# Kernel tuning notes

Measured on AMD Instinct MI355X. Metric: run time of the kernel, lower is better.

Reference implementation:

```python
import jax, jax.numpy as jnp
import numpy as np

B, T, A, F_, D, H = 8, 128, 6, 64, 64, 4  # batch, time, antennas, subcarriers, d_model, heads


def setup_inputs() -> dict:
    key = jax.random.key(0)
    ks = jax.random.split(key, 10)
    d = D
    s = 1.0 / np.sqrt(d)
    return {
        "x": jax.random.normal(ks[0], (B, T, A, F_), jnp.float32),
        "embed_w": jax.random.normal(ks[1], (d, 1), jnp.float32) * 0.5,
        "embed_b": jax.random.normal(ks[2], (d,), jnp.float32) * 0.1,
        "in_proj_w": jax.random.normal(ks[3], (3 * d, d), jnp.float32) * s,
        "in_proj_b": jax.random.normal(ks[4], (3 * d,), jnp.float32) * 0.1,
        "out_proj_w": jax.random.normal(ks[5], (d, d), jnp.float32) * s,
        "out_proj_b": jax.random.normal(ks[6], (d,), jnp.float32) * 0.1,
        "ln_g": jnp.ones((d,), jnp.float32),
        "ln_b": jnp.zeros((d,), jnp.float32),
        "out_w": jax.random.normal(ks[7], (1, d), jnp.float32) * s,
        "out_b": jax.random.normal(ks[8], (1,), jnp.float32) * 0.1,
    }


def reference(x, embed_w, embed_b, in_proj_w, in_proj_b, out_proj_w,
              out_proj_b, ln_g, ln_b, out_w, out_b):
    b, t, a, f = x.shape
    d = embed_w.shape[0]
    h = H
    hd = d // h
    # [B,T,A,F] -> [B*T*F, A, 1]: each subcarrier becomes a 6-token sequence
    xf = jnp.transpose(x, (0, 1, 3, 2)).reshape(b * t * f, a, 1)
    hid = xf @ embed_w.T + embed_b  # [N, A, D]
    # combined in-projection like torch MultiheadAttention
    qkv = hid @ in_proj_w.T + in_proj_b  # [N, A, 3D]
    q, k, v = jnp.split(qkv, 3, axis=-1)
    q = q.reshape(-1, a, h, hd)
    k = k.reshape(-1, a, h, hd)
    v = v.reshape(-1, a, h, hd)
    scale = 1.0 / np.sqrt(hd)
    # diagonal -inf mask: a token cannot attend to itself
    mask = jnp.where(jnp.eye(a, dtype=bool), -jnp.inf, 0.0).astype(x.dtype)
    scores = jnp.einsum('nqhd,nkhd->nhqk', q, k) * scale + mask
    attn = jax.nn.softmax(scores, axis=-1)
    o = jnp.einsum('nhqk,nkhd->nqhd', attn, v).reshape(-1, a, d)
    o = o @ out_proj_w.T + out_proj_b
    # residual + LayerNorm (eps=1e-5, torch default)
    y = o + hid
    mu = jnp.mean(y, axis=-1, keepdims=True)
    var = jnp.var(y, axis=-1, keepdims=True)
    y = (y - mu) / jnp.sqrt(var + 1e-5) * ln_g + ln_b
    y = y @ out_w.T + out_b  # [N, A, 1]
    return jnp.transpose(y.reshape(b, t, f, a), (0, 1, 3, 2))
```

## Files before the change

kernel.cpp:

```cpp
#include <hip/hip_runtime.h>
#include <hip/hip_bf16.h>
#include <math.h>


#define DD 64

__global__ void sca_precompute(
    const float* __restrict__ embed_w,
    const float* __restrict__ embed_b,
    const float* __restrict__ in_proj_w,
    const float* __restrict__ in_proj_b,
    const float* __restrict__ out_proj_w,
    const float* __restrict__ out_proj_b,
    const float* __restrict__ ln_g,
    const float* __restrict__ ln_b,
    const float* __restrict__ out_w,
    const float* __restrict__ out_b,
    float* __restrict__ K)
{
    __shared__ float wqkv[192];
    __shared__ float cqkv[192];
    __shared__ float Mc[6][DD];
    __shared__ float mcol[6];

    const int tid = threadIdx.x;

    if (tid < 192) {
        float sw = 0.f, sc = 0.f;
        #pragma unroll
        for (int e = 0; e < DD; ++e) {
            float wrow = in_proj_w[tid * DD + e];
            sw += wrow * embed_w[e];
            sc += wrow * embed_b[e];
        }
        wqkv[tid] = sw;
        cqkv[tid] = sc + in_proj_b[tid];
    }
    __syncthreads();

    if (tid < 4) {
        const float scale = 0.25f;
        float a = 0.f, bb = 0.f, c = 0.f, d = 0.f;
        #pragma unroll
        for (int k = 0; k < 16; ++k) {
            int qd = tid * 16 + k;
            float wq = wqkv[qd],      cq = cqkv[qd];
            float wk = wqkv[64 + qd], ck = cqkv[64 + qd];
            a  += wq * wk;
            bb += wq * ck;
            c  += cq * wk;
            d  += cq * ck;
        }
        K[0 + tid]  = a  * scale;
        K[4 + tid]  = bb * scale;
        K[8 + tid]  = c  * scale;
        K[12 + tid] = d  * scale;
    }

    if (tid < DD) {
        int d = tid;
        #pragma unroll
        for (int h = 0; h < 4; ++h) {
            float s = 0.f;
            #pragma unroll
            for (int k = 0; k < 16; ++k) {
                int e = h * 16 + k;
                s += out_proj_w[d * DD + e] * wqkv[128 + e];
            }
            Mc[h][d] = s;
        }
        float c0 = out_proj_b[d];
        #pragma unroll
        for (int e = 0; e < DD; ++e)
            c0 += out_proj_w[d * DD + e] * cqkv[128 + e];
        Mc[4][d] = embed_w[d];
        Mc[5][d] = c0 + embed_b[d];
    }
    __syncthreads();

    if (tid < 6) {
        float s = 0.f;
        for (int d = 0; d < DD; ++d) s += Mc[tid][d];
        mcol[tid] = s * (1.f / DD);
    }
    __syncthreads();

    if (tid < DD) {
        #pragma unroll
        for (int j = 0; j < 6; ++j) Mc[j][tid] -= mcol[j];
    }
    __syncthreads();

    if (tid < 36) {
        int j = tid / 6, k2 = tid % 6;
        float s = 0.f;
        for (int d = 0; d < DD; ++d) s += Mc[j][d] * Mc[k2][d];
        K[22 + tid] = s * (1.f / DD);
    } else if (tid < 42) {
        int j = tid - 36;
        float s = 0.f;
        for (int d = 0; d < DD; ++d) s += out_w[d] * ln_g[d] * Mc[j][d];
        K[16 + j] = s;
    } else if (tid == 42) {
        float s = out_b[0];
        for (int d = 0; d < DD; ++d) s += out_w[d] * ln_b[d];
        K[58] = s;
    }
}

__global__ __launch_bounds__(256) void sca_main(
    const float* __restrict__ x,
    const float* __restrict__ K,
    float* __restrict__ out,
    int N)
{
    int n = blockIdx.x * blockDim.x + threadIdx.x;
    if (n >= N) return;

    const int base = (n >> 6) * 384 + (n & 63);

    float xv[6];
    #pragma unroll
    for (int a = 0; a < 6; ++a) xv[a] = x[base + (a << 6)];

    float s[6][4];
    #pragma unroll
    for (int h = 0; h < 4; ++h) {
        const float ah = K[h], bh = K[4 + h], ch = K[8 + h], dh = K[12 + h];
        float fj[6], gj[6];
        #pragma unroll
        for (int j = 0; j < 6; ++j) {
            fj[j] = ah * xv[j] + bh;
            gj[j] = ch * xv[j] + dh;
        }
        #pragma unroll
        for (int i = 0; i < 6; ++i) {
            float sc[6];
            float mx = -1e30f;
            #pragma unroll
            for (int j = 0; j < 6; ++j) {
                if (j == i) continue;
                sc[j] = xv[i] * fj[j] + gj[j];
                mx = fmaxf(mx, sc[j]);
            }
            float Z = 0.f, sv = 0.f;
            #pragma unroll
            for (int j = 0; j < 6; ++j) {
                if (j == i) continue;
                float e = __expf(sc[j] - mx);
                Z += e;
                sv += e * xv[j];
            }
            s[i][h] = sv / Z;
        }
    }

    float pc[6];
    #pragma unroll
    for (int j = 0; j < 6; ++j) pc[j] = K[16 + j];
    float Gc[6][6];
    #pragma unroll
    for (int j = 0; j < 36; ++j) Gc[j / 6][j % 6] = K[22 + j];
    const float C = K[58];

    #pragma unroll
    for (int i = 0; i < 6; ++i) {
        float t[6] = { s[i][0], s[i][1], s[i][2], s[i][3], xv[i], 1.f };
        float num = 0.f, var = 0.f;
        #pragma unroll
        for (int j = 0; j < 6; ++j) {
            num += pc[j] * t[j];
            float rv = 0.f;
            #pragma unroll
            for (int k = 0; k < 6; ++k) rv += Gc[j][k] * t[k];
            var += rv * t[j];
        }
        out[base + (i << 6)] = num * rsqrtf(var + 1e-5f) + C;
    }
}

extern "C" void kernel_launch(void* const* d_in, const int* in_sizes, int n_in,
                              void* d_out, int out_size, void* d_ws, size_t ws_size,
                              hipStream_t stream) {
    const float* x          = (const float*)d_in[0];
    const float* embed_w    = (const float*)d_in[1];
    const float* embed_b    = (const float*)d_in[2];
    const float* in_proj_w  = (const float*)d_in[3];
    const float* in_proj_b  = (const float*)d_in[4];
    const float* out_proj_w = (const float*)d_in[5];
    const float* out_proj_b = (const float*)d_in[6];
    const float* ln_g       = (const float*)d_in[7];
    const float* ln_b       = (const float*)d_in[8];
    const float* out_w      = (const float*)d_in[9];
    const float* out_b      = (const float*)d_in[10];

    float* K = (float*)d_ws;
    float* out = (float*)d_out;

    const int N = in_sizes[0] / 6;

    sca_precompute<<<1, 192, 0, stream>>>(embed_w, embed_b, in_proj_w, in_proj_b,
                                          out_proj_w, out_proj_b, ln_g, ln_b,
                                          out_w, out_b, K);

    const int block = 256;
    const int grid = (N + block - 1) / block;
    sca_main<<<grid, block, 0, stream>>>(x, K, out, N);
}
```

Measured before the change: 85.07 us.

## Fuse weight precompute into main kernel and exploit Gram matrix symmetry

Removes the single-block precompute launch and has every block redundantly fold the weights into constants in shared memory before the per-sequence attention and LayerNorm math. This drops one kernel launch and its serialization, at the cost of every block repeating the folding work (192 threads each reading a 64-wide row of in_proj_w, plus the out_proj loops) before it can start. It also stores only the 21 upper-triangle Gram coefficients with doubled off-diagonals, which shrinks the variance quadratic form.

```diff
diff --git a/kernel.cpp b/kernel.cpp
--- a/kernel.cpp
+++ b/kernel.cpp
@@ -5,7 +5,8 @@
 
 #define DD 64
 
-__global__ void sca_precompute(
+__global__ __launch_bounds__(256) void sca_fused(
+    const float* __restrict__ x,
     const float* __restrict__ embed_w,
     const float* __restrict__ embed_b,
     const float* __restrict__ in_proj_w,
@@ -16,12 +17,14 @@
     const float* __restrict__ ln_b,
     const float* __restrict__ out_w,
     const float* __restrict__ out_b,
-    float* __restrict__ K)
+    float* __restrict__ out,
+    int N)
 {
     __shared__ float wqkv[192];
     __shared__ float cqkv[192];
     __shared__ float Mc[6][DD];
     __shared__ float mcol[6];
+    __shared__ float sK[44];
 
     const int tid = threadIdx.x;
 
@@ -29,9 +32,9 @@
         float sw = 0.f, sc = 0.f;
         #pragma unroll
         for (int e = 0; e < DD; ++e) {
-            float wrow = in_proj_w[tid * DD + e];
-            sw += wrow * embed_w[e];
-            sc += wrow * embed_b[e];
+            float wr = in_proj_w[tid * DD + e];
+            sw += wr * embed_w[e];
+            sc += wr * embed_b[e];
         }
         wqkv[tid] = sw;
         cqkv[tid] = sc + in_proj_b[tid];
@@ -51,10 +54,10 @@
             c  += cq * wk;
             d  += cq * ck;
         }
-        K[0 + tid]  = a  * scale;
-        K[4 + tid]  = bb * scale;
-        K[8 + tid]  = c  * scale;
-        K[12 + tid] = d  * scale;
+        sK[0 + tid]  = a  * scale;
+        sK[4 + tid]  = bb * scale;
+        sK[8 + tid]  = c  * scale;
+        sK[12 + tid] = d  * scale;
     }
 
     if (tid < DD) {
@@ -91,30 +94,26 @@
     }
     __syncthreads();
 
-    if (tid < 36) {
-        int j = tid / 6, k2 = tid % 6;
+    if (tid < 21) {
+        int j = 0, rr = tid;
+        while (rr > 5 - j) { rr -= (6 - j); ++j; }
+        int k = j + rr;
         float s = 0.f;
-        for (int d = 0; d < DD; ++d) s += Mc[j][d] * Mc[k2][d];
-        K[22 + tid] = s * (1.f / DD);
-    } else if (tid < 42) {
-        int j = tid - 36;
+        for (int d = 0; d < DD; ++d) s += Mc[j][d] * Mc[k][d];
+        sK[22 + tid] = s * (1.f / DD) * (j == k ? 1.f : 2.f);
+    } else if (tid < 27) {
+        int j = tid - 21;
         float s = 0.f;
         for (int d = 0; d < DD; ++d) s += out_w[d] * ln_g[d] * Mc[j][d];
-        K[16 + j] = s;
-    } else if (tid == 42) {
+        sK[16 + j] = s;
+    } else if (tid == 27) {
         float s = out_b[0];
         for (int d = 0; d < DD; ++d) s += out_w[d] * ln_b[d];
-        K[58] = s;
-    }
-}
-
-__global__ __launch_bounds__(256) void sca_main(
-    const float* __restrict__ x,
-    const float* __restrict__ K,
-    float* __restrict__ out,
-    int N)
-{
-    int n = blockIdx.x * blockDim.x + threadIdx.x;
+        sK[43] = s;
+    }
+    __syncthreads();
+
+    const int n = blockIdx.x * 256 + tid;
     if (n >= N) return;
 
     const int base = (n >> 6) * 384 + (n & 63);
@@ -123,15 +122,28 @@
     #pragma unroll
     for (int a = 0; a < 6; ++a) xv[a] = x[base + (a << 6)];
 
+    float ka[4], kb[4], kc[4], kd[4];
+    #pragma unroll
+    for (int h = 0; h < 4; ++h) {
+        ka[h] = sK[h];      kb[h] = sK[4 + h];
+        kc[h] = sK[8 + h];  kd[h] = sK[12 + h];
+    }
+    float pcv[6];
+    #pragma unroll
+    for (int j = 0; j < 6; ++j) pcv[j] = sK[16 + j];
+    float G2[21];
+    #pragma unroll
+    for (int r = 0; r < 21; ++r) G2[r] = sK[22 + r];
+    const float C = sK[43];
+
     float s[6][4];
     #pragma unroll
     for (int h = 0; h < 4; ++h) {
-        const float ah = K[h], bh = K[4 + h], ch = K[8 + h], dh = K[12 + h];
         float fj[6], gj[6];
         #pragma unroll
         for (int j = 0; j < 6; ++j) {
-            fj[j] = ah * xv[j] + bh;
-            gj[j] = ch * xv[j] + dh;
+            fj[j] = ka[h] * xv[j] + kb[h];
+            gj[j] = kc[h] * xv[j] + kd[h];
         }
         #pragma unroll
         for (int i = 0; i < 6; ++i) {
@@ -155,25 +167,18 @@
         }
     }
 
-    float pc[6];
-    #pragma unroll
-    for (int j = 0; j < 6; ++j) pc[j] = K[16 + j];
-    float Gc[6][6];
-    #pragma unroll
-    for (int j = 0; j < 36; ++j) Gc[j / 6][j % 6] = K[22 + j];
-    const float C = K[58];
-
     #pragma unroll
     for (int i = 0; i < 6; ++i) {
         float t[6] = { s[i][0], s[i][1], s[i][2], s[i][3], xv[i], 1.f };
         float num = 0.f, var = 0.f;
+        int idx = 0;
         #pragma unroll
         for (int j = 0; j < 6; ++j) {
-            num += pc[j] * t[j];
-            float rv = 0.f;
-            #pragma unroll
-            for (int k = 0; k < 6; ++k) rv += Gc[j][k] * t[k];
-            var += rv * t[j];
+            num += pcv[j] * t[j];
+            #pragma unroll
+            for (int k = j; k < 6; ++k) {
+                var += G2[idx++] * t[j] * t[k];
+            }
         }
         out[base + (i << 6)] = num * rsqrtf(var + 1e-5f) + C;
     }
@@ -194,16 +199,12 @@
     const float* out_w      = (const float*)d_in[9];
     const float* out_b      = (const float*)d_in[10];
 
-    float* K = (float*)d_ws;
     float* out = (float*)d_out;
-
     const int N = in_sizes[0] / 6;
-
-    sca_precompute<<<1, 192, 0, stream>>>(embed_w, embed_b, in_proj_w, in_proj_b,
-                                          out_proj_w, out_proj_b, ln_g, ln_b,
-                                          out_w, out_b, K);
 
     const int block = 256;
     const int grid = (N + block - 1) / block;
-    sca_main<<<grid, block, 0, stream>>>(x, K, out, N);
+    sca_fused<<<grid, block, 0, stream>>>(x, embed_w, embed_b, in_proj_w,
+                                          in_proj_b, out_proj_w, out_proj_b,
+                                          ln_g, ln_b, out_w, out_b, out, N);
 }
```

Result: no change. 84.11 us (-1.1%).
